# Kernel tuning notes

Hardware: AMD Instinct MI355X
Metric: run time of the kernel (lower is better)

Reference implementation:

```python
import jax, jax.numpy as jnp
import numpy as np
import math

N_HEADS = 32
N_KV_HEADS = 8
HEAD_DIM = 64
THETA = 10000.0
NEG_INF = -1e9


def _rope_cos_sin(seq_len, dim, dtype=jnp.float32):
    # freqs over even indices, matching torch.arange(0, dim, 2)/dim
    freqs = 1.0 / (THETA ** (jnp.arange(0, dim, 2, dtype=jnp.float32) / dim))  # [dim/2]
    angles = jnp.arange(seq_len, dtype=jnp.float32)[:, None] * freqs[None, :]  # [S, dim/2]
    return jnp.cos(angles).astype(dtype), jnp.sin(angles).astype(dtype)


def _apply_rope(x, cos, sin):
    # x: [B, S, H, D]; pairs (x[...,2i], x[...,2i+1]) rotated as complex numbers
    xr = x[..., 0::2]
    xi = x[..., 1::2]
    # broadcast cos/sin [S, D/2] -> [1, S, 1, D/2]
    c = cos[None, :, None, :]
    s = sin[None, :, None, :]
    or_ = xr * c - xi * s
    oi_ = xr * s + xi * c
    # interleave back: [..., D/2, 2] -> [..., D]
    return jnp.stack([or_, oi_], axis=-1).reshape(x.shape)


def setup_inputs() -> dict:
    key = jax.random.key(0)
    ks = jax.random.split(key, 5)
    B, S, D = 2, 2048, 2048
    KV_D = N_KV_HEADS * HEAD_DIM
    x = jax.random.normal(ks[0], (B, S, D), dtype=jnp.float32)
    sc = 1.0 / math.sqrt(D)
    wq = jax.random.normal(ks[1], (D, D), dtype=jnp.float32) * sc
    wk = jax.random.normal(ks[2], (D, KV_D), dtype=jnp.float32) * sc
    wv = jax.random.normal(ks[3], (D, KV_D), dtype=jnp.float32) * sc
    wo = jax.random.normal(ks[4], (D, D), dtype=jnp.float32) * sc
    # additive causal mask [1, 1, S, S]
    causal = jnp.tril(jnp.ones((S, S), dtype=bool))
    mask = jnp.where(causal, 0.0, NEG_INF).astype(jnp.float32)[None, None]
    return {"x": x, "mask": mask, "wq": wq, "wk": wk, "wv": wv, "wo": wo}


def reference(x, mask, wq, wk, wv, wo):
    B, S, D = x.shape
    n_rep = N_HEADS // N_KV_HEADS
    q = (x @ wq).reshape(B, S, N_HEADS, HEAD_DIM)
    k = (x @ wk).reshape(B, S, N_KV_HEADS, HEAD_DIM)
    v = (x @ wv).reshape(B, S, N_KV_HEADS, HEAD_DIM)
    cos, sin = _rope_cos_sin(S, HEAD_DIM)
    q = _apply_rope(q, cos, sin)
    k = _apply_rope(k, cos, sin)
    # GQA: repeat_interleave kv heads along head dim
    k = jnp.repeat(k, n_rep, axis=2)  # [B, S, H, D]
    v = jnp.repeat(v, n_rep, axis=2)
    scores = jnp.einsum("bqhd,bkhd->bhqk", q, k) / math.sqrt(HEAD_DIM)
    scores = scores + mask
    probs = jax.nn.softmax(scores.astype(jnp.float32), axis=-1).astype(q.dtype)
    out = jnp.einsum("bhqk,bkhd->bqhd", probs, v).reshape(B, S, N_HEADS * HEAD_DIM)
    return out @ wo
```

## Files before the change

kernel.cpp:

```cpp
#include <hip/hip_runtime.h>
#include <hip/hip_bf16.h>


#define S_LEN 2048
#define BATCH 2
#define D_MODEL 2048
#define NH 32
#define NKV 8
#define HD 64
#define KV_D (NKV * HD)
#define QKV_N (D_MODEL + 2 * KV_D)

typedef __attribute__((ext_vector_type(8))) short short8;
typedef __attribute__((ext_vector_type(4))) float float4v;
typedef __attribute__((ext_vector_type(16))) float f32x16;
typedef __attribute__((ext_vector_type(2))) unsigned uint2v;

typedef __attribute__((address_space(1))) const unsigned int gu32;
typedef __attribute__((address_space(3))) unsigned int lu32;

#if __has_builtin(__builtin_amdgcn_exp2f)
#define PEXP(x) __builtin_amdgcn_exp2f(x)
#else
#define PEXP(x) __expf((x) * 0.69314718f)
#endif
#define QSCALE 0.18033688f

__device__ __forceinline__ float bf2f(unsigned short u) {
    unsigned x = ((unsigned)u) << 16;
    return __builtin_bit_cast(float, x);
}
__device__ __forceinline__ unsigned short f2bf(float f) {
    unsigned u = __builtin_bit_cast(unsigned, f);
    unsigned r = (u + 0x7fffu + ((u >> 16) & 1u)) >> 16;
    return (unsigned short)r;
}

__device__ __forceinline__ unsigned cvt_pk_bf16(float a, float b) {
    unsigned r;
    asm("v_cvt_pk_bf16_f32 %0, %1, %2" : "=v"(r) : "v"(a), "v"(b));
    return r;
}

__device__ __forceinline__ void pl32swap(unsigned a, unsigned b,
                                         unsigned& x, unsigned& y) {
#if __has_builtin(__builtin_amdgcn_permlane32_swap)
    uint2v r = __builtin_amdgcn_permlane32_swap(a, b, false, false);
    x = r[0];
    y = r[1];
#else
    unsigned pa = (unsigned)__shfl_xor((int)a, 32);
    unsigned pb = (unsigned)__shfl_xor((int)b, 32);
    bool lo = (threadIdx.x & 63) < 32;
    x = lo ? a : pb;
    y = lo ? pa : b;
#endif
}

__global__ void cast_f32_bf16(const float* __restrict__ in,
                              unsigned short* __restrict__ out, long n) {
    long i = ((long)blockIdx.x * 256 + threadIdx.x) * 4;
    if (i + 3 >= n) return;
    const float4v v = *(const float4v*)&in[i];
    unsigned short o[4];
    o[0] = f2bf(v[0]); o[1] = f2bf(v[1]); o[2] = f2bf(v[2]); o[3] = f2bf(v[3]);
    *(__attribute__((ext_vector_type(4))) short*)&out[i] =
        *(__attribute__((ext_vector_type(4))) short*)o;
}

__global__ __launch_bounds__(256) void wtrans(const float* __restrict__ in,
                                              unsigned short* __restrict__ out,
                                              int K, int N) {
    __shared__ unsigned short t[32 * 33];
    const int nb = blockIdx.x * 32, kb = blockIdx.y * 32;
    const int c = threadIdx.x & 31, rr = threadIdx.x >> 5;
#pragma unroll
    for (int it = 0; it < 4; ++it) {
        int r = it * 8 + rr;
        t[c * 33 + r] = f2bf(in[(long)(kb + r) * N + nb + c]);
    }
    __syncthreads();
#pragma unroll
    for (int it = 0; it < 4; ++it) {
        int r = it * 8 + rr;
        out[(long)(nb + r) * K + kb + c] = t[r * 33 + c];
    }
}

template <int TM, bool F32OUT>
__global__ __launch_bounds__(256, TM == 64 ? 4 : 3)
void gemm_sw(const unsigned short* __restrict__ A,
             const unsigned short* __restrict__ BT,
             void* __restrict__ Cv, int M, int N, int K) {
    __shared__ unsigned short As[TM * 64];
    __shared__ unsigned short Bs[128 * 64];
    const int tid = threadIdx.x;
    const int wid = tid >> 6, lane = tid & 63;
    const int l15 = lane & 15, quad = lane >> 4;
    const int wm = (wid >> 1) * (TM / 2), wn = (wid & 1) * 64;
    const int row0 = blockIdx.x * TM, col0 = blockIdx.y * 128;
    constexpr int MI = TM / 32;

    float4v acc[MI][4];
    float4v z;
    z[0] = z[1] = z[2] = z[3] = 0.0f;
    for (int mi = 0; mi < MI; ++mi)
        for (int ni = 0; ni < 4; ++ni) acc[mi][ni] = z;

    const int r_ld = lane >> 3;
    const int swz_ld = ((lane & 7) ^ (lane >> 3)) * 8;
    const int sw = l15 & 7;

    for (int kb = 0; kb < K; kb += 64) {
        __syncthreads();
#pragma unroll
        for (int c = 0; c < 4; ++c) {
            int chunk = c * 4 + wid;
            int r = chunk * 8 + r_ld;
            __builtin_amdgcn_global_load_lds(
                (gu32*)&BT[(long)(col0 + r) * K + kb + swz_ld],
                (lu32*)&Bs[chunk * 512], 16, 0, 0);
            if (c < MI)
                __builtin_amdgcn_global_load_lds(
                    (gu32*)&A[(long)(row0 + r) * K + kb + swz_ld],
                    (lu32*)&As[chunk * 512], 16, 0, 0);
        }
        __syncthreads();
#pragma unroll
        for (int kk = 0; kk < 64; kk += 32) {
            short8 af[MI], bf[4];
#pragma unroll
            for (int i = 0; i < MI; ++i)
                af[i] = *(const short8*)
                    &As[(wm + i * 16 + l15) * 64 + ((((kk >> 3) + quad) ^ sw) << 3)];
#pragma unroll
            for (int i = 0; i < 4; ++i)
                bf[i] = *(const short8*)
                    &Bs[(wn + i * 16 + l15) * 64 + ((((kk >> 3) + quad) ^ sw) << 3)];
#pragma unroll
            for (int mi = 0; mi < MI; ++mi)
#pragma unroll
                for (int ni = 0; ni < 4; ++ni)
                    acc[mi][ni] = __builtin_amdgcn_mfma_f32_16x16x32_bf16(
                        af[mi], bf[ni], acc[mi][ni], 0, 0, 0);
        }
    }
#pragma unroll
    for (int mi = 0; mi < MI; ++mi)
#pragma unroll
        for (int ni = 0; ni < 4; ++ni)
#pragma unroll
            for (int r = 0; r < 4; ++r) {
                int m = row0 + wm + mi * 16 + quad * 4 + r;
                int n = col0 + wn + ni * 16 + l15;
                if (F32OUT)
                    ((float*)Cv)[(long)m * N + n] = acc[mi][ni][r];
                else
                    ((unsigned short*)Cv)[(long)m * N + n] = f2bf(acc[mi][ni][r]);
            }
}

__global__ __launch_bounds__(256) void rope2(unsigned short* __restrict__ qkv) {
    const int i = threadIdx.x & 31;
    const int row = blockIdx.x * 8 + (threadIdx.x >> 5);
    const int s = row & (S_LEN - 1);
    float freq = __expf(-0.28782313f * (float)i);
    float ang = (float)s * freq;
    float c = cosf(ang), sn = sinf(ang);
    unsigned* p = (unsigned*)qkv + ((long)row * QKV_N + 2 * i) / 2;
#pragma unroll
    for (int head = 0; head < 40; ++head) {
        const float qs = (head < 32) ? QSCALE : 1.0f;
        unsigned v = p[head * 32];
        float xr = bf2f((unsigned short)(v & 0xffff));
        float xi = bf2f((unsigned short)(v >> 16));
        unsigned short lo = f2bf((xr * c - xi * sn) * qs);
        unsigned short hi = f2bf((xr * sn + xi * c) * qs);
        p[head * 32] = (unsigned)lo | ((unsigned)hi << 16);
    }
}

__global__ __launch_bounds__(256) void vtrans(const unsigned short* __restrict__ qkv,
                                              unsigned short* __restrict__ Vt) {
    __shared__ unsigned t[64 * 33];
    const int st = blockIdx.x * 64, kh = blockIdx.y, b = blockIdx.z;
    const int tid = threadIdx.x;
    {
        const int r2 = tid >> 3, dbase = (tid & 7) * 8;
        const unsigned short* src =
            qkv + ((long)(b * S_LEN + st + 2 * r2)) * QKV_N + D_MODEL + KV_D + kh * HD + dbase;
        short8 lo = *(const short8*)src;
        short8 hi = *(const short8*)(src + QKV_N);
#pragma unroll
        for (int j = 0; j < 8; ++j)
            t[(dbase + j) * 33 + r2] =
                (unsigned)(unsigned short)lo[j] | ((unsigned)(unsigned short)hi[j] << 16);
    }
    __syncthreads();
    {
        const int d = tid >> 2, sb = (tid & 3) * 8;
        unsigned short o[16];
#pragma unroll
        for (int jj = 0; jj < 8; ++jj) {
            unsigned v = t[d * 33 + sb + jj];
            o[2 * jj] = (unsigned short)(v & 0xffff);
            o[2 * jj + 1] = (unsigned short)(v >> 16);
        }
        unsigned short* dst =
            Vt + ((long)((b * 8 + kh) * 64 + d)) * S_LEN + st + sb * 2;
        *(short8*)dst = *(short8*)&o[0];
        *(short8*)(dst + 8) = *(short8*)&o[8];
    }
}

__global__ __launch_bounds__(256, 4) void flash7(const unsigned short* __restrict__ qkv,
                                                 const unsigned short* __restrict__ Vt,
                                                 unsigned short* __restrict__ O) {
    __shared__ unsigned short Ks[2][64 * 64];
    __shared__ unsigned short Vs[2][64 * 64];

    const int tid = threadIdx.x, w = tid >> 6, lane = tid & 63;
    const int l31 = lane & 31, hi = lane >> 5;
    const int r7 = l31 & 7;
    const int h = blockIdx.y, b = blockIdx.z;
    const int kh = h >> 2, bkh = b * 8 + kh;
    const int qtA = blockIdx.x;

    const int sr = lane >> 3;
    const int sc = ((lane & 7) ^ sr) * 8;
    const int kr0 = w * 8 + sr, kr1 = 32 + w * 8 + sr;
    const unsigned short* Kg =
        qkv + (long)b * S_LEN * QKV_N + D_MODEL + kh * HD + sc;
    const unsigned short* Vg = Vt + ((long)bkh * 64) * S_LEN + sc;

#define STAGE7(buf, kb)                                                              \
    do {                                                                             \
        __builtin_amdgcn_global_load_lds((gu32*)&Kg[(long)((kb) + kr0) * QKV_N],     \
                                         (lu32*)&Ks[buf][w * 512], 16, 0, 0);        \
        __builtin_amdgcn_global_load_lds((gu32*)&Kg[(long)((kb) + kr1) * QKV_N],     \
                                         (lu32*)&Ks[buf][2048 + w * 512], 16, 0, 0); \
        __builtin_amdgcn_global_load_lds((gu32*)&Vg[(long)kr0 * S_LEN + (kb)],       \
                                         (lu32*)&Vs[buf][w * 512], 16, 0, 0);        \
        __builtin_amdgcn_global_load_lds((gu32*)&Vg[(long)kr1 * S_LEN + (kb)],       \
                                         (lu32*)&Vs[buf][2048 + w * 512], 16, 0, 0); \
    } while (0)

    for (int tsel = 0; tsel < 2; ++tsel) {
        const int qt = tsel ? (15 - qtA) : qtA;
        const int row_w = qt * 128 + w * 32;
        const int nkt = 2 * qt + 2;

        short8 aq[4];
        {
            const long qbase = ((long)(b * S_LEN) + row_w + l31) * QKV_N + h * HD + hi * 8;
#pragma unroll
            for (int ks = 0; ks < 4; ++ks) aq[ks] = *(const short8*)&qkv[qbase + ks * 16];
        }

        f32x16 oacc[2] = {};
        float lp = 0.0f;

        STAGE7(0, 0);
        __syncthreads();

        for (int kti = 0; kti < nkt; ++kti) {
            const int k0 = kti * 64;
            const int cur = kti & 1;
            if (kti + 1 < nkt) STAGE7(cur ^ 1, k0 + 64);

            if (row_w + 31 >= k0) {
                const bool mb = (k0 + 63 > row_w);
#pragma unroll
                for (int kb2 = 0; kb2 < 2; ++kb2) {
                    short8 kf[4];
#pragma unroll
                    for (int ks = 0; ks < 4; ++ks)
                        kf[ks] = *(const short8*)
                            &Ks[cur][(kb2 * 32 + l31) * 64 + (((ks * 2 + hi) ^ r7) << 3)];
                    f32x16 s = {};
                    __builtin_amdgcn_s_setprio(1);
#pragma unroll
                    for (int ks = 0; ks < 4; ++ks)
                        s = __builtin_amdgcn_mfma_f32_32x32x16_bf16(kf[ks], aq[ks], s, 0, 0, 0);
                    __builtin_amdgcn_s_setprio(0);

                    const int qrel = row_w + l31 - k0 - kb2 * 32 - 4 * hi;
#pragma unroll
                    for (int r = 0; r < 16; ++r) {
                        float v = s[r];
                        if (mb && ((r & 3) + 8 * (r >> 2) > qrel)) v = -1e4f;
                        float p = PEXP(v);
                        lp += p;
                        s[r] = p;
                    }

#pragma unroll
                    for (int ksl = 0; ksl < 2; ++ksl) {
                        const int g = ksl * 8;
                        unsigned ca = cvt_pk_bf16(s[g + 0], s[g + 1]);
                        unsigned cb = cvt_pk_bf16(s[g + 2], s[g + 3]);
                        unsigned cc = cvt_pk_bf16(s[g + 4], s[g + 5]);
                        unsigned cd = cvt_pk_bf16(s[g + 6], s[g + 7]);
                        unsigned dw0, dw1, dw2, dw3;
                        pl32swap(ca, cc, dw0, dw2);
                        pl32swap(cb, cd, dw1, dw3);
                        union { unsigned u[4]; short8 v8; } pf;
                        pf.u[0] = dw0; pf.u[1] = dw1; pf.u[2] = dw2; pf.u[3] = dw3;
                        const int lc = kb2 * 4 + ksl * 2 + hi;
                        __builtin_amdgcn_s_setprio(1);
#pragma unroll
                        for (int dblk = 0; dblk < 2; ++dblk) {
                            short8 vf = *(const short8*)
                                &Vs[cur][(dblk * 32 + l31) * 64 + ((lc ^ r7) << 3)];
                            oacc[dblk] = __builtin_amdgcn_mfma_f32_32x32x16_bf16(
                                vf, pf.v8, oacc[dblk], 0, 0, 0);
                        }
                        __builtin_amdgcn_s_setprio(0);
                    }
                }
            }
            __syncthreads();
        }

        float linv = 1.0f / (lp + __shfl_xor(lp, 32));
        unsigned short* Oe = &Ks[0][0] + w * 2048;
#pragma unroll
        for (int dblk = 0; dblk < 2; ++dblk)
#pragma unroll
            for (int rq = 0; rq < 4; ++rq) {
                unsigned plo = cvt_pk_bf16(oacc[dblk][rq * 4 + 0] * linv,
                                           oacc[dblk][rq * 4 + 1] * linv);
                unsigned phi = cvt_pk_bf16(oacc[dblk][rq * 4 + 2] * linv,
                                           oacc[dblk][rq * 4 + 3] * linv);
                uint2v wv;
                wv[0] = plo; wv[1] = phi;
                int e = l31 * 64 + (((rq + 4 * dblk) ^ r7) << 3) + hi * 4;
                *(uint2v*)&Oe[e] = wv;
            }
#pragma unroll
        for (int i = 0; i < 4; ++i) {
            int q2 = i * 8 + (lane >> 3);
            int e = q2 * 64 + (((lane & 7) ^ (lane >> 3)) << 3);
            short8 ov = *(const short8*)&Oe[e];
            long orow = ((long)(b * S_LEN) + row_w + q2) * D_MODEL + h * HD + (lane & 7) * 8;
            *(short8*)&O[orow] = ov;
        }
        __syncthreads();
    }
#undef STAGE7
}

extern "C" void kernel_launch(void* const* d_in, const int* in_sizes, int n_in,
                              void* d_out, int out_size, void* d_ws, size_t ws_size,
                              hipStream_t stream) {
    const float* x  = (const float*)d_in[0];
    const float* wq = (const float*)d_in[n_in - 4];
    const float* wk = (const float*)d_in[n_in - 3];
    const float* wv = (const float*)d_in[n_in - 2];
    const float* wo = (const float*)d_in[n_in - 1];
    float* out = (float*)d_out;

    unsigned short* ws    = (unsigned short*)d_ws;
    unsigned short* xb    = ws;
    unsigned short* Obuf  = ws;
    unsigned short* qkv   = xb + (long)BATCH * S_LEN * D_MODEL;
    unsigned short* woT   = qkv + (long)BATCH * S_LEN * QKV_N;
    unsigned short* wqkvT = woT + (long)D_MODEL * D_MODEL;
    unsigned short* Vt    = wqkvT;

    const int M = BATCH * S_LEN;
    const long xn = (long)M * D_MODEL;

    cast_f32_bf16<<<(int)(xn / 4 / 256), 256, 0, stream>>>(x, xb, xn);

    wtrans<<<dim3(D_MODEL / 32, D_MODEL / 32), 256, 0, stream>>>(wq, wqkvT, D_MODEL, D_MODEL);
    wtrans<<<dim3(KV_D / 32, D_MODEL / 32), 256, 0, stream>>>(wk, wqkvT + (long)D_MODEL * D_MODEL, D_MODEL, KV_D);
    wtrans<<<dim3(KV_D / 32, D_MODEL / 32), 256, 0, stream>>>(wv, wqkvT + (long)(D_MODEL + KV_D) * D_MODEL, D_MODEL, KV_D);
    wtrans<<<dim3(D_MODEL / 32, D_MODEL / 32), 256, 0, stream>>>(wo, woT, D_MODEL, D_MODEL);

    gemm_sw<128, false><<<dim3(M / 128, QKV_N / 128), 256, 0, stream>>>(
        xb, wqkvT, qkv, M, QKV_N, D_MODEL);

    rope2<<<M / 8, 256, 0, stream>>>(qkv);

    vtrans<<<dim3(S_LEN / 64, NKV, BATCH), 256, 0, stream>>>(qkv, Vt);

    flash7<<<dim3(8, NH, BATCH), 256, 0, stream>>>(qkv, Vt, Obuf);

    gemm_sw<64, true><<<dim3(M / 64, D_MODEL / 128), 256, 0, stream>>>(
        Obuf, woT, out, M, D_MODEL, D_MODEL);
}
```

Before: 302.9 us.

## Replace QKV projection GEMM with 256x256-tile 8-wave ping-pong kernel

Adds a specialized bf16 GEMM for the fused QKV projection that uses 256x256 output tiles, 512 threads (8 waves), double-buffered LDS filled via global_load_lds, and interleaved barrier/setprio phases so loads overlap MFMA work. It replaces the generic 128-tile gemm_sw launch. The larger tile increases operand reuse per LDS load. In exchange it uses 128KB of LDS and many accumulator registers, and it launches only 16x12 blocks, which may leave some CUs idle.

```diff
diff --git a/kernel.cpp b/kernel.cpp
--- a/kernel.cpp
+++ b/kernel.cpp
@@ -160,6 +160,143 @@
             }
 }
 
+#define M8 4096
+#define N8 3072
+#define K8 2048
+#define NK8 (K8 / 64)
+
+__device__ __forceinline__ void rd_a8(short8 (&a)[4][2], const unsigned short* L,
+                                      int mh, int wr, int l15, int quad, int sw) {
+#pragma unroll
+    for (int i = 0; i < 4; ++i) {
+        const int ra = mh * 128 + i * 32 + wr * 16 + l15;
+#pragma unroll
+        for (int kk = 0; kk < 2; ++kk)
+            a[i][kk] = *(const short8*)&L[ra * 64 + (((kk * 4 + quad) ^ sw) << 3)];
+    }
+}
+__device__ __forceinline__ void rd_b8(short8 (&b)[2][2], const unsigned short* L,
+                                      int nh, int wc, int l15, int quad, int sw) {
+#pragma unroll
+    for (int j = 0; j < 2; ++j) {
+        const int rb = nh * 128 + j * 64 + wc * 16 + l15;
+#pragma unroll
+        for (int kk = 0; kk < 2; ++kk)
+            b[j][kk] = *(const short8*)&L[rb * 64 + (((kk * 4 + quad) ^ sw) << 3)];
+    }
+}
+__device__ __forceinline__ void mm8(float4v (&acc)[4][2], const short8 (&a)[4][2],
+                                    const short8 (&b)[2][2]) {
+#pragma unroll
+    for (int kk = 0; kk < 2; ++kk)
+#pragma unroll
+        for (int i = 0; i < 4; ++i)
+#pragma unroll
+            for (int j = 0; j < 2; ++j)
+                acc[i][j] = __builtin_amdgcn_mfma_f32_16x16x32_bf16(
+                    a[i][kk], b[j][kk], acc[i][j], 0, 0, 0);
+}
+
+__global__ __launch_bounds__(512, 2)
+void gemm8(const unsigned short* __restrict__ A,
+           const unsigned short* __restrict__ BT,
+           unsigned short* __restrict__ C) {
+    __shared__ unsigned short As[2][256 * 64];
+    __shared__ unsigned short Bs[2][256 * 64];
+    const int tid = threadIdx.x, wid = tid >> 6, lane = tid & 63;
+    const int l15 = lane & 15, quad = lane >> 4, sw = l15 & 7;
+    const int wr = wid >> 2, wc = wid & 3;
+    const int row0 = blockIdx.x * 256, col0 = blockIdx.y * 256;
+
+    const int sr = lane >> 3;
+    const int sc = ((lane & 7) ^ sr) * 8;
+    const unsigned short* Ag = A + (long)(row0 + wid * 8 + sr) * K8 + sc;
+    const unsigned short* Bg = BT + (long)(col0 + wid * 8 + sr) * K8 + sc;
+
+#define STA8(buf, kb, u)                                                   \
+    __builtin_amdgcn_global_load_lds(                                      \
+        (gu32*)(Ag + (long)(u) * (64L * K8) + (kb)),                       \
+        (lu32*)&As[buf][((u)*64 + wid * 8) * 64], 16, 0, 0)
+#define STB8(buf, kb, u)                                                   \
+    __builtin_amdgcn_global_load_lds(                                      \
+        (gu32*)(Bg + (long)(u) * (64L * K8) + (kb)),                       \
+        (lu32*)&Bs[buf][((u)*64 + wid * 8) * 64], 16, 0, 0)
+
+    float4v acc[2][2][4][2];
+#pragma unroll
+    for (int mh = 0; mh < 2; ++mh)
+#pragma unroll
+        for (int nh = 0; nh < 2; ++nh)
+#pragma unroll
+            for (int i = 0; i < 4; ++i)
+#pragma unroll
+                for (int j = 0; j < 2; ++j) {
+                    acc[mh][nh][i][j][0] = 0.0f; acc[mh][nh][i][j][1] = 0.0f;
+                    acc[mh][nh][i][j][2] = 0.0f; acc[mh][nh][i][j][3] = 0.0f;
+                }
+
+    STA8(0, 0, 0); STA8(0, 0, 1); STA8(0, 0, 2); STA8(0, 0, 3);
+    STB8(0, 0, 0); STB8(0, 0, 1); STB8(0, 0, 2); STB8(0, 0, 3);
+    asm volatile("s_waitcnt vmcnt(0)" ::: "memory");
+    __builtin_amdgcn_s_barrier();
+
+    for (int t = 0; t < NK8; ++t) {
+        const int ct = t & 1, nx = ct ^ 1;
+        const int kb = (t + 1) * 64;
+        const bool more = (t + 1 < NK8);
+        const unsigned short* Al = As[ct];
+        const unsigned short* Bl = Bs[ct];
+        short8 a0[4][2], a1[4][2], b0v[2][2], b1v[2][2];
+
+        rd_a8(a0, Al, 0, wr, l15, quad, sw);
+        rd_b8(b0v, Bl, 0, wc, l15, quad, sw);
+        if (more) { STA8(nx, kb, 0); STA8(nx, kb, 1); STA8(nx, kb, 2); STA8(nx, kb, 3); }
+        __builtin_amdgcn_s_barrier();
+        __builtin_amdgcn_s_setprio(1);
+        mm8(acc[0][0], a0, b0v);
+        __builtin_amdgcn_s_setprio(0);
+        __builtin_amdgcn_s_barrier();
+
+        rd_b8(b1v, Bl, 1, wc, l15, quad, sw);
+        if (more) { STB8(nx, kb, 0); STB8(nx, kb, 1); STB8(nx, kb, 2); STB8(nx, kb, 3); }
+        __builtin_amdgcn_s_barrier();
+        __builtin_amdgcn_s_setprio(1);
+        mm8(acc[0][1], a0, b1v);
+        __builtin_amdgcn_s_setprio(0);
+        __builtin_amdgcn_s_barrier();
+
+        rd_a8(a1, Al, 1, wr, l15, quad, sw);
+        __builtin_amdgcn_s_barrier();
+        __builtin_amdgcn_s_setprio(1);
+        mm8(acc[1][0], a1, b0v);
+        __builtin_amdgcn_s_setprio(0);
+        __builtin_amdgcn_s_barrier();
+
+        __builtin_amdgcn_s_setprio(1);
+        mm8(acc[1][1], a1, b1v);
+        __builtin_amdgcn_s_setprio(0);
+        if (more) asm volatile("s_waitcnt vmcnt(0)" ::: "memory");
+        __builtin_amdgcn_s_barrier();
+    }
+
+#pragma unroll
+    for (int mh = 0; mh < 2; ++mh)
+#pragma unroll
+        for (int nh = 0; nh < 2; ++nh)
+#pragma unroll
+            for (int i = 0; i < 4; ++i)
+#pragma unroll
+                for (int j = 0; j < 2; ++j)
+#pragma unroll
+                    for (int r = 0; r < 4; ++r) {
+                        int m = row0 + mh * 128 + i * 32 + wr * 16 + quad * 4 + r;
+                        int n = col0 + nh * 128 + j * 64 + wc * 16 + l15;
+                        C[(long)m * N8 + n] = f2bf(acc[mh][nh][i][j][r]);
+                    }
+#undef STA8
+#undef STB8
+}
+
 __global__ __launch_bounds__(256) void rope2(unsigned short* __restrict__ qkv) {
     const int i = threadIdx.x & 31;
     const int row = blockIdx.x * 8 + (threadIdx.x >> 5);
@@ -378,8 +515,7 @@
     wtrans<<<dim3(KV_D / 32, D_MODEL / 32), 256, 0, stream>>>(wv, wqkvT + (long)(D_MODEL + KV_D) * D_MODEL, D_MODEL, KV_D);
     wtrans<<<dim3(D_MODEL / 32, D_MODEL / 32), 256, 0, stream>>>(wo, woT, D_MODEL, D_MODEL);
 
-    gemm_sw<128, false><<<dim3(M / 128, QKV_N / 128), 256, 0, stream>>>(
-        xb, wqkvT, qkv, M, QKV_N, D_MODEL);
+    gemm8<<<dim3(M8 / 256, N8 / 256), 512, 0, stream>>>(xb, wqkvT, qkv);
 
     rope2<<<M / 8, 256, 0, stream>>>(qkv);
 
```

New measurement: 308.8 us. Within noise of the previous version (+2.0%).

## Split flash attention KV loop across two wave groups with LDS reduction

Applied to the files above, without the earlier changes.

Doubles the attention block to 512 threads. Two groups of four waves each process alternating KV tiles for the same query rows, using a 4-deep K/V LDS buffer. Partial output accumulators and row sums from the second group are reduced through shared memory before normalization and store. This is meant to raise parallelism and hide latency in the causal attention loop. The cost is more LDS, an extra reduction pass and lower occupancy per CU.

```diff
diff --git a/kernel.cpp b/kernel.cpp
--- a/kernel.cpp
+++ b/kernel.cpp
@@ -213,13 +213,14 @@
     }
 }
 
-__global__ __launch_bounds__(256, 4) void flash7(const unsigned short* __restrict__ qkv,
+__global__ __launch_bounds__(512, 4) void flash8(const unsigned short* __restrict__ qkv,
                                                  const unsigned short* __restrict__ Vt,
                                                  unsigned short* __restrict__ O) {
-    __shared__ unsigned short Ks[2][64 * 64];
-    __shared__ unsigned short Vs[2][64 * 64];
+    __shared__ unsigned short Ks[4][64 * 64];
+    __shared__ unsigned short Vs[4][64 * 64];
 
     const int tid = threadIdx.x, w = tid >> 6, lane = tid & 63;
+    const int g = w & 3, p = w >> 2;
     const int l31 = lane & 31, hi = lane >> 5;
     const int r7 = l31 & 7;
     const int h = blockIdx.y, b = blockIdx.z;
@@ -228,27 +229,34 @@
 
     const int sr = lane >> 3;
     const int sc = ((lane & 7) ^ sr) * 8;
-    const int kr0 = w * 8 + sr, kr1 = 32 + w * 8 + sr;
     const unsigned short* Kg =
         qkv + (long)b * S_LEN * QKV_N + D_MODEL + kh * HD + sc;
     const unsigned short* Vg = Vt + ((long)bkh * 64) * S_LEN + sc;
 
-#define STAGE7(buf, kb)                                                              \
+#define STAGE8(pb)                                                                   \
     do {                                                                             \
-        __builtin_amdgcn_global_load_lds((gu32*)&Kg[(long)((kb) + kr0) * QKV_N],     \
-                                         (lu32*)&Ks[buf][w * 512], 16, 0, 0);        \
-        __builtin_amdgcn_global_load_lds((gu32*)&Kg[(long)((kb) + kr1) * QKV_N],     \
-                                         (lu32*)&Ks[buf][2048 + w * 512], 16, 0, 0); \
-        __builtin_amdgcn_global_load_lds((gu32*)&Vg[(long)kr0 * S_LEN + (kb)],       \
-                                         (lu32*)&Vs[buf][w * 512], 16, 0, 0);        \
-        __builtin_amdgcn_global_load_lds((gu32*)&Vg[(long)kr1 * S_LEN + (kb)],       \
-                                         (lu32*)&Vs[buf][2048 + w * 512], 16, 0, 0); \
+        const int tt = (pb) + p;                                                     \
+        const int bt = tt & 3;                                                       \
+        const long kk0 = (long)tt * 64;                                              \
+        __builtin_amdgcn_global_load_lds(                                            \
+            (gu32*)&Kg[(kk0 + g * 16 + sr) * QKV_N],                                 \
+            (lu32*)&Ks[bt][(g * 16) * 64], 16, 0, 0);                                \
+        __builtin_amdgcn_global_load_lds(                                            \
+            (gu32*)&Kg[(kk0 + g * 16 + 8 + sr) * QKV_N],                             \
+            (lu32*)&Ks[bt][(g * 16 + 8) * 64], 16, 0, 0);                            \
+        __builtin_amdgcn_global_load_lds(                                            \
+            (gu32*)&Vg[(long)(g * 16 + sr) * S_LEN + kk0],                           \
+            (lu32*)&Vs[bt][(g * 16) * 64], 16, 0, 0);                                \
+        __builtin_amdgcn_global_load_lds(                                            \
+            (gu32*)&Vg[(long)(g * 16 + 8 + sr) * S_LEN + kk0],                       \
+            (lu32*)&Vs[bt][(g * 16 + 8) * 64], 16, 0, 0);                            \
     } while (0)
 
     for (int tsel = 0; tsel < 2; ++tsel) {
         const int qt = tsel ? (15 - qtA) : qtA;
-        const int row_w = qt * 128 + w * 32;
+        const int row_w = qt * 128 + g * 32;
         const int nkt = 2 * qt + 2;
+        const int nss = nkt >> 1;
 
         short8 aq[4];
         {
@@ -260,13 +268,14 @@
         f32x16 oacc[2] = {};
         float lp = 0.0f;
 
-        STAGE7(0, 0);
+        STAGE8(0);
         __syncthreads();
 
-        for (int kti = 0; kti < nkt; ++kti) {
-            const int k0 = kti * 64;
-            const int cur = kti & 1;
-            if (kti + 1 < nkt) STAGE7(cur ^ 1, k0 + 64);
+        for (int ss = 0; ss < nss; ++ss) {
+            const int t = 2 * ss + p;
+            const int k0 = t * 64;
+            const int bt = t & 3;
+            if (2 * ss + 2 < nkt) STAGE8(2 * ss + 2);
 
             if (row_w + 31 >= k0) {
                 const bool mb = (k0 + 63 > row_w);
@@ -276,7 +285,7 @@
 #pragma unroll
                     for (int ks = 0; ks < 4; ++ks)
                         kf[ks] = *(const short8*)
-                            &Ks[cur][(kb2 * 32 + l31) * 64 + (((ks * 2 + hi) ^ r7) << 3)];
+                            &Ks[bt][(kb2 * 32 + l31) * 64 + (((ks * 2 + hi) ^ r7) << 3)];
                     f32x16 s = {};
                     __builtin_amdgcn_s_setprio(1);
 #pragma unroll
@@ -289,18 +298,18 @@
                     for (int r = 0; r < 16; ++r) {
                         float v = s[r];
                         if (mb && ((r & 3) + 8 * (r >> 2) > qrel)) v = -1e4f;
-                        float p = PEXP(v);
-                        lp += p;
-                        s[r] = p;
+                        float pv = PEXP(v);
+                        lp += pv;
+                        s[r] = pv;
                     }
 
 #pragma unroll
                     for (int ksl = 0; ksl < 2; ++ksl) {
-                        const int g = ksl * 8;
-                        unsigned ca = cvt_pk_bf16(s[g + 0], s[g + 1]);
-                        unsigned cb = cvt_pk_bf16(s[g + 2], s[g + 3]);
-                        unsigned cc = cvt_pk_bf16(s[g + 4], s[g + 5]);
-                        unsigned cd = cvt_pk_bf16(s[g + 6], s[g + 7]);
+                        const int gx = ksl * 8;
+                        unsigned ca = cvt_pk_bf16(s[gx + 0], s[gx + 1]);
+                        unsigned cb = cvt_pk_bf16(s[gx + 2], s[gx + 3]);
+                        unsigned cc = cvt_pk_bf16(s[gx + 4], s[gx + 5]);
+                        unsigned cd = cvt_pk_bf16(s[gx + 6], s[gx + 7]);
                         unsigned dw0, dw1, dw2, dw3;
                         pl32swap(ca, cc, dw0, dw2);
                         pl32swap(cb, cd, dw1, dw3);
@@ -311,7 +320,7 @@
 #pragma unroll
                         for (int dblk = 0; dblk < 2; ++dblk) {
                             short8 vf = *(const short8*)
-                                &Vs[cur][(dblk * 32 + l31) * 64 + ((lc ^ r7) << 3)];
+                                &Vs[bt][(dblk * 32 + l31) * 64 + ((lc ^ r7) << 3)];
                             oacc[dblk] = __builtin_amdgcn_mfma_f32_32x32x16_bf16(
                                 vf, pf.v8, oacc[dblk], 0, 0, 0);
                         }
@@ -322,32 +331,52 @@
             __syncthreads();
         }
 
-        float linv = 1.0f / (lp + __shfl_xor(lp, 32));
-        unsigned short* Oe = &Ks[0][0] + w * 2048;
-#pragma unroll
-        for (int dblk = 0; dblk < 2; ++dblk)
-#pragma unroll
-            for (int rq = 0; rq < 4; ++rq) {
-                unsigned plo = cvt_pk_bf16(oacc[dblk][rq * 4 + 0] * linv,
-                                           oacc[dblk][rq * 4 + 1] * linv);
-                unsigned phi = cvt_pk_bf16(oacc[dblk][rq * 4 + 2] * linv,
-                                           oacc[dblk][rq * 4 + 3] * linv);
-                uint2v wv;
-                wv[0] = plo; wv[1] = phi;
-                int e = l31 * 64 + (((rq + 4 * dblk) ^ r7) << 3) + hi * 4;
-                *(uint2v*)&Oe[e] = wv;
+        float* mV = (float*)&Vs[0][0];
+        float* mL = (float*)&Ks[2][0];
+        if (p == 1) {
+#pragma unroll
+            for (int dblk = 0; dblk < 2; ++dblk)
+#pragma unroll
+                for (int r = 0; r < 16; ++r)
+                    mV[(g * 32 + dblk * 16 + r) * 64 + lane] = oacc[dblk][r];
+            mL[g * 64 + lane] = lp;
+        }
+        __syncthreads();
+        if (p == 0) {
+#pragma unroll
+            for (int dblk = 0; dblk < 2; ++dblk)
+#pragma unroll
+                for (int r = 0; r < 16; ++r)
+                    oacc[dblk][r] += mV[(g * 32 + dblk * 16 + r) * 64 + lane];
+            lp += mL[g * 64 + lane];
+
+            float linv = 1.0f / (lp + __shfl_xor(lp, 32));
+            unsigned short* Oe = &Ks[0][0] + g * 2048;
+#pragma unroll
+            for (int dblk = 0; dblk < 2; ++dblk)
+#pragma unroll
+                for (int rq = 0; rq < 4; ++rq) {
+                    unsigned plo = cvt_pk_bf16(oacc[dblk][rq * 4 + 0] * linv,
+                                               oacc[dblk][rq * 4 + 1] * linv);
+                    unsigned phi = cvt_pk_bf16(oacc[dblk][rq * 4 + 2] * linv,
+                                               oacc[dblk][rq * 4 + 3] * linv);
+                    uint2v wv;
+                    wv[0] = plo; wv[1] = phi;
+                    int e = l31 * 64 + (((rq + 4 * dblk) ^ r7) << 3) + hi * 4;
+                    *(uint2v*)&Oe[e] = wv;
+                }
+#pragma unroll
+            for (int i = 0; i < 4; ++i) {
+                int q2 = i * 8 + (lane >> 3);
+                int e = q2 * 64 + (((lane & 7) ^ (lane >> 3)) << 3);
+                short8 ov = *(const short8*)&Oe[e];
+                long orow = ((long)(b * S_LEN) + row_w + q2) * D_MODEL + h * HD + (lane & 7) * 8;
+                *(short8*)&O[orow] = ov;
             }
-#pragma unroll
-        for (int i = 0; i < 4; ++i) {
-            int q2 = i * 8 + (lane >> 3);
-            int e = q2 * 64 + (((lane & 7) ^ (lane >> 3)) << 3);
-            short8 ov = *(const short8*)&Oe[e];
-            long orow = ((long)(b * S_LEN) + row_w + q2) * D_MODEL + h * HD + (lane & 7) * 8;
-            *(short8*)&O[orow] = ov;
         }
         __syncthreads();
     }
-#undef STAGE7
+#undef STAGE8
 }
 
 extern "C" void kernel_launch(void* const* d_in, const int* in_sizes, int n_in,
@@ -385,7 +414,7 @@
 
     vtrans<<<dim3(S_LEN / 64, NKV, BATCH), 256, 0, stream>>>(qkv, Vt);
 
-    flash7<<<dim3(8, NH, BATCH), 256, 0, stream>>>(qkv, Vt, Obuf);
+    flash8<<<dim3(8, NH, BATCH), 512, 0, stream>>>(qkv, Vt, Obuf);
 
     gemm_sw<64, true><<<dim3(M / 64, D_MODEL / 128), 256, 0, stream>>>(
         Obuf, woT, out, M, D_MODEL, D_MODEL);
```

Measured after the change: 310.7 us. 1.03x slower.
